# Performance work log

Hardware: AMD Instinct MI355X
Metric: run time of the kernel (lower is better)

## Reference

```python
import jax, jax.numpy as jnp
import numpy as np


def setup_inputs() -> dict:
    key = jax.random.key(0)
    ks = jax.random.split(key, 7)
    B, T, D, H, C = 256, 512, 128, 512, 10
    s_ih = 1.0 / np.sqrt(H)
    return {
        "X": jax.random.normal(ks[0], (B, T, D), dtype=jnp.float32),
        "W_ih": jax.random.normal(ks[1], (4 * H, D), dtype=jnp.float32) * s_ih,
        "W_hh": jax.random.normal(ks[2], (4 * H, H), dtype=jnp.float32) * s_ih,
        "b_ih": jax.random.normal(ks[3], (4 * H,), dtype=jnp.float32) * s_ih,
        "b_hh": jax.random.normal(ks[4], (4 * H,), dtype=jnp.float32) * s_ih,
        "W_lin": jax.random.normal(ks[5], (C, H), dtype=jnp.float32) * s_ih,
        "b_lin": jax.random.normal(ks[6], (C,), dtype=jnp.float32) * s_ih,
    }


def _lstm_mean_h(X, W_ih, W_hh, b_ih, b_hh):
    B, T, D = X.shape
    H = W_hh.shape[1]
    # Input projections for all timesteps at once: [T, B, 4H]
    x_proj = jnp.einsum("btd,kd->tbk", X, W_ih) + b_ih + b_hh

    def step(carry, xp):
        h, c = carry
        gates = xp + h @ W_hh.T  # [B, 4H]
        i, f, g, o = jnp.split(gates, 4, axis=-1)  # PyTorch i,f,g,o order
        i = jax.nn.sigmoid(i)
        f = jax.nn.sigmoid(f)
        g = jnp.tanh(g)
        o = jax.nn.sigmoid(o)
        c = f * c + i * g
        h = o * jnp.tanh(c)
        return (h, c), h

    h0 = jnp.zeros((B, H), dtype=X.dtype)
    (_, _), hs = jax.lax.scan(step, (h0, h0), x_proj)  # hs: [T, B, H]
    return jnp.mean(hs, axis=0)  # == sum(h_t)/T


def reference(X, W_ih, W_hh, b_ih, b_hh, W_lin, b_lin):
    states = _lstm_mean_h(X, W_ih, W_hh, b_ih, b_hh)  # [B, H]
    logits = states @ W_lin.T + b_lin  # [B, num_classes]
    return logits
```

## Files before the change

kernel.cpp:

```cpp
#include <hip/hip_runtime.h>
#include <stdint.h>


#define T_STEPS 512
#define BATCH   256
#define DIM     128
#define HID     512
#define NGRP    16
#define BT      16

typedef _Float16 half8 __attribute__((ext_vector_type(8)));
typedef _Float16 half4 __attribute__((ext_vector_type(4)));
typedef float    f32x4 __attribute__((ext_vector_type(4)));

#define HBUF_HALFS (2 * BATCH * HID)
#define FLG_OFF    (HBUF_HALFS * 2)
#define WS_NEEDED  (FLG_OFF + NGRP * 128)

__device__ __forceinline__ half8 cvt8(f32x4 a, f32x4 b) {
  half8 r;
  r[0]=(_Float16)a[0]; r[1]=(_Float16)a[1]; r[2]=(_Float16)a[2]; r[3]=(_Float16)a[3];
  r[4]=(_Float16)b[0]; r[5]=(_Float16)b[1]; r[6]=(_Float16)b[2]; r[7]=(_Float16)b[3];
  return r;
}
__device__ __forceinline__ half8 load8_cvt(const float* p) {
  const f32x4* q = (const f32x4*)p;
  return cvt8(q[0], q[1]);
}
__device__ __forceinline__ float fsig(float x) {
  return __builtin_amdgcn_rcpf(1.f + __expf(-x));
}
__device__ __forceinline__ float ftanh(float x) {
  return 1.f - 2.f * __builtin_amdgcn_rcpf(1.f + __expf(2.f * x));
}

union h4u { unsigned long long u; half4 h; };
union h8u { unsigned long long u2[2]; half8 h; };

__global__ __launch_bounds__(256, 1) void lstm_persistent(
    const float* __restrict__ X,   const float* __restrict__ Wih,
    const float* __restrict__ Whh, const float* __restrict__ bih,
    const float* __restrict__ bhh, const float* __restrict__ Wlin,
    float* __restrict__ out, _Float16* __restrict__ hbuf,
    unsigned* __restrict__ flg)
{
  const int tid  = threadIdx.x;
  const int w    = tid >> 6;
  const int lane = tid & 63;
  const int col  = lane & 15;
  const int q    = lane >> 4;
  const int bid  = blockIdx.x;
  const int g    = bid & 15;
  const int blk  = bid >> 4;
  const int J    = blk * 64 + w * 16;
  const int wid  = blk * 4 + w;
  const int b_my = g * BT + col;

  half8 whh[16][4];
  half8 wih[4][4];
  #pragma unroll
  for (int kc = 0; kc < 16; ++kc)
    #pragma unroll
    for (int mt = 0; mt < 4; ++mt) {
      const int row = mt * HID + J + col;
      whh[kc][mt] = load8_cvt(Whh + (size_t)row * HID + kc * 32 + q * 8);
    }
  #pragma unroll
  for (int xc = 0; xc < 4; ++xc)
    #pragma unroll
    for (int mt = 0; mt < 4; ++mt) {
      const int row = mt * HID + J + col;
      wih[xc][mt] = load8_cvt(Wih + (size_t)row * DIM + xc * 32 + q * 8);
    }

  float bias[4][4], c_st[4], hsum[4];
  #pragma unroll
  for (int mt = 0; mt < 4; ++mt)
    #pragma unroll
    for (int r = 0; r < 4; ++r) {
      const int row = mt * HID + J + q * 4 + r;
      bias[mt][r] = bih[row] + bhh[row];
    }
  #pragma unroll
  for (int r = 0; r < 4; ++r) { c_st[r] = 0.f; hsum[r] = 0.f; }

  unsigned* myflg = flg + g * 32;
  const float* Xb = X + (size_t)b_my * T_STEPS * DIM;

  f32x4 xraw[8];
  #pragma unroll
  for (int xc = 0; xc < 4; ++xc) {
    const f32x4* p = (const f32x4*)(Xb + xc * 32 + q * 8);
    xraw[2 * xc] = p[0]; xraw[2 * xc + 1] = p[1];
  }
  f32x4 acc[4];
  #pragma unroll
  for (int mt = 0; mt < 4; ++mt) acc[mt] = (f32x4){0.f, 0.f, 0.f, 0.f};
  #pragma unroll
  for (int xc = 0; xc < 4; ++xc) {
    half8 xb = cvt8(xraw[2 * xc], xraw[2 * xc + 1]);
    #pragma unroll
    for (int mt = 0; mt < 4; ++mt)
      acc[mt] = __builtin_amdgcn_mfma_f32_16x16x32_f16(wih[xc][mt], xb, acc[mt], 0, 0, 0);
  }

  for (int t = 0; t < T_STEPS; ++t) {
    {
      const int tn = (t + 1 < T_STEPS) ? (t + 1) : (T_STEPS - 1);
      const float* xp = Xb + (size_t)tn * DIM + q * 8;
      #pragma unroll
      for (int xc = 0; xc < 4; ++xc) {
        const f32x4* src = (const f32x4*)(xp + xc * 32);
        xraw[2 * xc]     = src[0];
        xraw[2 * xc + 1] = src[1];
      }
    }

    if (t > 0) {
      const unsigned target = (unsigned)t;
      for (;;) {
        unsigned v = __hip_atomic_load(myflg + (lane & 31), __ATOMIC_RELAXED,
                                       __HIP_MEMORY_SCOPE_AGENT);
        if (__all((int)(v >= target))) break;
      }
      __builtin_amdgcn_sched_barrier(0);

      const unsigned long long* hp =
          (const unsigned long long*)(hbuf + (size_t)(t & 1) * (BATCH * HID)
                                      + (size_t)b_my * HID) + q * 2;
      unsigned long long lo[16], hi[16];
      #pragma unroll
      for (int kc = 0; kc < 16; ++kc) {
        lo[kc] = __hip_atomic_load(hp + kc * 8,     __ATOMIC_RELAXED, __HIP_MEMORY_SCOPE_AGENT);
        hi[kc] = __hip_atomic_load(hp + kc * 8 + 1, __ATOMIC_RELAXED, __HIP_MEMORY_SCOPE_AGENT);
      }
      #pragma unroll
      for (int kc = 0; kc < 16; ++kc) {
        h8u u; u.u2[0] = lo[kc]; u.u2[1] = hi[kc];
        #pragma unroll
        for (int mt = 0; mt < 4; ++mt)
          acc[mt] = __builtin_amdgcn_mfma_f32_16x16x32_f16(whh[kc][mt], u.h, acc[mt], 0, 0, 0);
      }
    }

    h4u hv;
    #pragma unroll
    for (int r = 0; r < 4; ++r) {
      const float ig = fsig(acc[0][r] + bias[0][r]);
      const float fg = fsig(acc[1][r] + bias[1][r]);
      const float gg = ftanh(acc[2][r] + bias[2][r]);
      const float og = fsig(acc[3][r] + bias[3][r]);
      const float cc = fg * c_st[r] + ig * gg;
      c_st[r] = cc;
      const float h = og * ftanh(cc);
      hsum[r] += h;
      hv.h[r] = (_Float16)h;
    }
    unsigned long long* hw =
        (unsigned long long*)(hbuf + (size_t)((t + 1) & 1) * (BATCH * HID)
                              + (size_t)b_my * HID + J + q * 4);
    __hip_atomic_store(hw, hv.u, __ATOMIC_RELAXED, __HIP_MEMORY_SCOPE_AGENT);

    if (t + 1 < T_STEPS) {
      asm volatile("s_waitcnt vmcnt(0)" ::: "memory");
      if (lane == 0)
        __hip_atomic_store(myflg + wid, (unsigned)(t + 1), __ATOMIC_RELAXED,
                           __HIP_MEMORY_SCOPE_AGENT);

      #pragma unroll
      for (int mt = 0; mt < 4; ++mt) acc[mt] = (f32x4){0.f, 0.f, 0.f, 0.f};
      #pragma unroll
      for (int xc = 0; xc < 4; ++xc) {
        half8 xb = cvt8(xraw[2 * xc], xraw[2 * xc + 1]);
        #pragma unroll
        for (int mt = 0; mt < 4; ++mt)
          acc[mt] = __builtin_amdgcn_mfma_f32_16x16x32_f16(wih[xc][mt], xb, acc[mt], 0, 0, 0);
      }
    }
  }

  const float inv = 1.0f / (float)T_STEPS;
  float m[4];
  #pragma unroll
  for (int r = 0; r < 4; ++r) m[r] = hsum[r] * inv;
  #pragma unroll
  for (int cls = 0; cls < 10; ++cls) {
    f32x4 wl = *(const f32x4*)(Wlin + (size_t)cls * HID + J + q * 4);
    float p = m[0] * wl[0] + m[1] * wl[1] + m[2] * wl[2] + m[3] * wl[3];
    p += __shfl_xor(p, 16, 64);
    p += __shfl_xor(p, 32, 64);
    if (q == 0) atomicAdd(out + b_my * 10 + cls, p);
  }
}

__global__ void init_out(const float* __restrict__ blin, float* __restrict__ out) {
  const int i = blockIdx.x * blockDim.x + threadIdx.x;
  if (i < BATCH * 10) out[i] = blin[i % 10];
}

extern "C" void kernel_launch(void* const* d_in, const int* in_sizes, int n_in,
                              void* d_out, int out_size, void* d_ws, size_t ws_size,
                              hipStream_t stream) {
  const float* X    = (const float*)d_in[0];
  const float* Wih  = (const float*)d_in[1];
  const float* Whh  = (const float*)d_in[2];
  const float* bih  = (const float*)d_in[3];
  const float* bhh  = (const float*)d_in[4];
  const float* Wlin = (const float*)d_in[5];
  const float* blin = (const float*)d_in[6];
  float* out = (float*)d_out;

  if (ws_size < (size_t)WS_NEEDED) return;

  _Float16* hbuf = (_Float16*)d_ws;
  unsigned* flg  = (unsigned*)((char*)d_ws + FLG_OFF);

  hipMemsetAsync(d_ws, 0, WS_NEEDED, stream);
  init_out<<<10, 256, 0, stream>>>(blin, out);
  lstm_persistent<<<128, 256, 0, stream>>>(X, Wih, Whh, bih, bhh, Wlin, out,
                                           hbuf, flg);
}
```

Baseline: 3.329 ms.

## Replace flag-based step sync with sentinel-tagged ring buffer of hidden states

```diff
diff --git a/kernel.cpp b/kernel.cpp
--- a/kernel.cpp
+++ b/kernel.cpp
@@ -8,14 +8,15 @@
 #define HID     512
 #define NGRP    16
 #define BT      16
+#define RBUF    8
 
 typedef _Float16 half8 __attribute__((ext_vector_type(8)));
 typedef _Float16 half4 __attribute__((ext_vector_type(4)));
 typedef float    f32x4 __attribute__((ext_vector_type(4)));
 
-#define HBUF_HALFS (2 * BATCH * HID)
-#define FLG_OFF    (HBUF_HALFS * 2)
-#define WS_NEEDED  (FLG_OFF + NGRP * 128)
+#define SLOT_HALFS (BATCH * HID)
+#define WS_NEEDED  (RBUF * SLOT_HALFS * 2)
+#define SENT       0x7F7F7F7F7F7F7F7FULL
 
 __device__ __forceinline__ half8 cvt8(f32x4 a, f32x4 b) {
   half8 r;
@@ -41,8 +42,7 @@
     const float* __restrict__ X,   const float* __restrict__ Wih,
     const float* __restrict__ Whh, const float* __restrict__ bih,
     const float* __restrict__ bhh, const float* __restrict__ Wlin,
-    float* __restrict__ out, _Float16* __restrict__ hbuf,
-    unsigned* __restrict__ flg)
+    float* __restrict__ out, _Float16* __restrict__ hbuf)
 {
   const int tid  = threadIdx.x;
   const int w    = tid >> 6;
@@ -53,7 +53,6 @@
   const int g    = bid & 15;
   const int blk  = bid >> 4;
   const int J    = blk * 64 + w * 16;
-  const int wid  = blk * 4 + w;
   const int b_my = g * BT + col;
 
   half8 whh[16][4];
@@ -84,8 +83,8 @@
   #pragma unroll
   for (int r = 0; r < 4; ++r) { c_st[r] = 0.f; hsum[r] = 0.f; }
 
-  unsigned* myflg = flg + g * 32;
   const float* Xb = X + (size_t)b_my * T_STEPS * DIM;
+  const size_t pub_off = (size_t)b_my * HID + J + q * 4;
 
   f32x4 xraw[8];
   #pragma unroll
@@ -116,24 +115,32 @@
       }
     }
 
+    {
+      unsigned long long* rp = (unsigned long long*)
+          (hbuf + (size_t)((t + 3) & (RBUF - 1)) * SLOT_HALFS + pub_off);
+      __hip_atomic_store(rp, (unsigned long long)SENT, __ATOMIC_RELAXED,
+                         __HIP_MEMORY_SCOPE_AGENT);
+    }
+
     if (t > 0) {
-      const unsigned target = (unsigned)t;
+      const unsigned long long* hp = (const unsigned long long*)
+          (hbuf + (size_t)(t & (RBUF - 1)) * SLOT_HALFS
+                 + (size_t)b_my * HID) + q * 2;
+      unsigned long long lo[16], hi[16];
       for (;;) {
-        unsigned v = __hip_atomic_load(myflg + (lane & 31), __ATOMIC_RELAXED,
-                                       __HIP_MEMORY_SCOPE_AGENT);
-        if (__all((int)(v >= target))) break;
+        #pragma unroll
+        for (int kc = 0; kc < 16; ++kc) {
+          lo[kc] = __hip_atomic_load(hp + kc * 8,     __ATOMIC_RELAXED, __HIP_MEMORY_SCOPE_AGENT);
+          hi[kc] = __hip_atomic_load(hp + kc * 8 + 1, __ATOMIC_RELAXED, __HIP_MEMORY_SCOPE_AGENT);
+        }
+        int ok = 1;
+        #pragma unroll
+        for (int kc = 0; kc < 16; ++kc)
+          ok &= (int)(lo[kc] != SENT) & (int)(hi[kc] != SENT);
+        if (__all(ok)) break;
       }
       __builtin_amdgcn_sched_barrier(0);
 
-      const unsigned long long* hp =
-          (const unsigned long long*)(hbuf + (size_t)(t & 1) * (BATCH * HID)
-                                      + (size_t)b_my * HID) + q * 2;
-      unsigned long long lo[16], hi[16];
-      #pragma unroll
-      for (int kc = 0; kc < 16; ++kc) {
-        lo[kc] = __hip_atomic_load(hp + kc * 8,     __ATOMIC_RELAXED, __HIP_MEMORY_SCOPE_AGENT);
-        hi[kc] = __hip_atomic_load(hp + kc * 8 + 1, __ATOMIC_RELAXED, __HIP_MEMORY_SCOPE_AGENT);
-      }
       #pragma unroll
       for (int kc = 0; kc < 16; ++kc) {
         h8u u; u.u2[0] = lo[kc]; u.u2[1] = hi[kc];
@@ -156,17 +163,15 @@
       hsum[r] += h;
       hv.h[r] = (_Float16)h;
     }
-    unsigned long long* hw =
-        (unsigned long long*)(hbuf + (size_t)((t + 1) & 1) * (BATCH * HID)
-                              + (size_t)b_my * HID + J + q * 4);
-    __hip_atomic_store(hw, hv.u, __ATOMIC_RELAXED, __HIP_MEMORY_SCOPE_AGENT);
+
+    asm volatile("s_waitcnt vmcnt(0)" ::: "memory");
+    {
+      unsigned long long* hw = (unsigned long long*)
+          (hbuf + (size_t)((t + 1) & (RBUF - 1)) * SLOT_HALFS + pub_off);
+      __hip_atomic_store(hw, hv.u, __ATOMIC_RELAXED, __HIP_MEMORY_SCOPE_AGENT);
+    }
 
     if (t + 1 < T_STEPS) {
-      asm volatile("s_waitcnt vmcnt(0)" ::: "memory");
-      if (lane == 0)
-        __hip_atomic_store(myflg + wid, (unsigned)(t + 1), __ATOMIC_RELAXED,
-                           __HIP_MEMORY_SCOPE_AGENT);
-
       #pragma unroll
       for (int mt = 0; mt < 4; ++mt) acc[mt] = (f32x4){0.f, 0.f, 0.f, 0.f};
       #pragma unroll
@@ -213,10 +218,9 @@
   if (ws_size < (size_t)WS_NEEDED) return;
 
   _Float16* hbuf = (_Float16*)d_ws;
-  unsigned* flg  = (unsigned*)((char*)d_ws + FLG_OFF);
-
-  hipMemsetAsync(d_ws, 0, WS_NEEDED, stream);
+
+  hipMemsetAsync(d_ws, 0x7F, WS_NEEDED, stream);
   init_out<<<10, 256, 0, stream>>>(blin, out);
   lstm_persistent<<<128, 256, 0, stream>>>(X, Wih, Whh, bih, bhh, Wlin, out,
-                                           hbuf, flg);
-}
+                                           hbuf);
+}
```

Measured after the change: 4.233 ms. 27.2% more time.

## Interleave two batch sub-groups per block to hide recurrent sync latency

Applied to the files above, without the earlier changes.

```diff
diff --git a/kernel.cpp b/kernel.cpp
--- a/kernel.cpp
+++ b/kernel.cpp
@@ -6,16 +6,15 @@
 #define BATCH   256
 #define DIM     128
 #define HID     512
-#define NGRP    16
-#define BT      16
+#define NGRP    8
 
 typedef _Float16 half8 __attribute__((ext_vector_type(8)));
-typedef _Float16 half4 __attribute__((ext_vector_type(4)));
 typedef float    f32x4 __attribute__((ext_vector_type(4)));
-
-#define HBUF_HALFS (2 * BATCH * HID)
-#define FLG_OFF    (HBUF_HALFS * 2)
-#define WS_NEEDED  (FLG_OFF + NGRP * 128)
+typedef float    f32x2 __attribute__((ext_vector_type(2)));
+
+#define SLOT_HALFS (BATCH * HID)
+#define FLG_OFF    (2 * SLOT_HALFS * 2)
+#define WS_NEEDED  (FLG_OFF + NGRP * 2 * 64 * 4)
 
 __device__ __forceinline__ half8 cvt8(f32x4 a, f32x4 b) {
   half8 r;
@@ -34,8 +33,113 @@
   return 1.f - 2.f * __builtin_amdgcn_rcpf(1.f + __expf(2.f * x));
 }
 
-union h4u { unsigned long long u; half4 h; };
+union h2u { unsigned u; _Float16 h[2]; };
 union h8u { unsigned long long u2[2]; half8 h; };
+
+template<int S>
+__device__ __forceinline__ void phase(
+    const int t, const int lane, const int q, const int J, const int wid,
+    const int bMy, const int bOth,
+    const half8 (&whh)[16][2], const half8 (&wih)[4][2],
+    const float (&bias)[2][4],
+    f32x4 (&acc)[2], float (&c_st)[2], float (&hsum)[2],
+    f32x4 (&xraw)[8], const float* __restrict__ Xb,
+    _Float16* __restrict__ hbuf,
+    unsigned* __restrict__ flgMine, unsigned* __restrict__ flgOth,
+    unsigned long long (&lo)[16], unsigned long long (&hi)[16])
+{
+  const int  tgt     = (S == 0) ? t : (t + 1);
+  const bool doPoll  = (S == 0) ? (t >= 1) : (t + 1 < T_STEPS);
+  const bool notLast = (t + 1 < T_STEPS);
+
+  unsigned ev = 0xFFFFFFFFu;
+  if (doPoll)
+    ev = __hip_atomic_load(flgOth + lane, __ATOMIC_RELAXED,
+                           __HIP_MEMORY_SCOPE_AGENT);
+
+  if (t > 0) {
+    #pragma unroll
+    for (int kc = 0; kc < 16; ++kc) {
+      h8u u; u.u2[0] = lo[kc]; u.u2[1] = hi[kc];
+      acc[0] = __builtin_amdgcn_mfma_f32_16x16x32_f16(whh[kc][0], u.h, acc[0], 0, 0, 0);
+      acc[1] = __builtin_amdgcn_mfma_f32_16x16x32_f16(whh[kc][1], u.h, acc[1], 0, 0, 0);
+    }
+  }
+
+  h2u hv;
+  {
+    const float i0 = fsig (acc[0][0] + bias[0][0]);
+    const float f0 = fsig (acc[0][1] + bias[0][1]);
+    const float g0 = ftanh(acc[1][0] + bias[1][0]);
+    const float o0 = fsig (acc[1][1] + bias[1][1]);
+    const float c0 = f0 * c_st[0] + i0 * g0;
+    c_st[0] = c0;
+    const float h0 = o0 * ftanh(c0);
+    hsum[0] += h0;
+    const float i1 = fsig (acc[0][2] + bias[0][2]);
+    const float f1 = fsig (acc[0][3] + bias[0][3]);
+    const float g1 = ftanh(acc[1][2] + bias[1][2]);
+    const float o1 = fsig (acc[1][3] + bias[1][3]);
+    const float c1 = f1 * c_st[1] + i1 * g1;
+    c_st[1] = c1;
+    const float h1 = o1 * ftanh(c1);
+    hsum[1] += h1;
+    hv.h[0] = (_Float16)h0; hv.h[1] = (_Float16)h1;
+  }
+
+  if (notLast) {
+    unsigned* hw = (unsigned*)(hbuf + (size_t)((t + 1) & 1) * SLOT_HALFS
+                               + (size_t)bMy * HID + J + 2 * q);
+    __hip_atomic_store(hw, hv.u, __ATOMIC_RELAXED, __HIP_MEMORY_SCOPE_AGENT);
+  }
+
+  if (doPoll) {
+    if (!__all((int)(ev >= (unsigned)tgt))) {
+      for (;;) {
+        unsigned v = __hip_atomic_load(flgOth + lane, __ATOMIC_RELAXED,
+                                       __HIP_MEMORY_SCOPE_AGENT);
+        if (__all((int)(v >= (unsigned)tgt))) break;
+      }
+    }
+    __builtin_amdgcn_sched_barrier(0);
+  }
+
+  if (notLast) {
+    asm volatile("s_waitcnt vmcnt(0)" ::: "memory");
+    if (lane == 0)
+      __hip_atomic_store(flgMine + wid, (unsigned)(t + 1), __ATOMIC_RELAXED,
+                         __HIP_MEMORY_SCOPE_AGENT);
+  }
+
+  if (doPoll) {
+    const unsigned long long* hp = (const unsigned long long*)
+        (hbuf + (size_t)(tgt & 1) * SLOT_HALFS + (size_t)bOth * HID) + q * 2;
+    #pragma unroll
+    for (int kc = 0; kc < 16; ++kc) {
+      lo[kc] = __hip_atomic_load(hp + kc * 8,     __ATOMIC_RELAXED, __HIP_MEMORY_SCOPE_AGENT);
+      hi[kc] = __hip_atomic_load(hp + kc * 8 + 1, __ATOMIC_RELAXED, __HIP_MEMORY_SCOPE_AGENT);
+    }
+  }
+
+  if (notLast) {
+    #pragma unroll
+    for (int mt = 0; mt < 2; ++mt) acc[mt] = (f32x4){0.f, 0.f, 0.f, 0.f};
+    #pragma unroll
+    for (int xc = 0; xc < 4; ++xc) {
+      half8 xb = cvt8(xraw[2 * xc], xraw[2 * xc + 1]);
+      acc[0] = __builtin_amdgcn_mfma_f32_16x16x32_f16(wih[xc][0], xb, acc[0], 0, 0, 0);
+      acc[1] = __builtin_amdgcn_mfma_f32_16x16x32_f16(wih[xc][1], xb, acc[1], 0, 0, 0);
+    }
+    const int tn = (t + 2 < T_STEPS) ? (t + 2) : (T_STEPS - 1);
+    const float* xp = Xb + (size_t)tn * DIM + q * 8;
+    #pragma unroll
+    for (int xc = 0; xc < 4; ++xc) {
+      const f32x4* src = (const f32x4*)(xp + xc * 32);
+      xraw[2 * xc]     = src[0];
+      xraw[2 * xc + 1] = src[1];
+    }
+  }
+}
 
 __global__ __launch_bounds__(256, 1) void lstm_persistent(
     const float* __restrict__ X,   const float* __restrict__ Wih,
@@ -50,146 +154,102 @@
   const int col  = lane & 15;
   const int q    = lane >> 4;
   const int bid  = blockIdx.x;
-  const int g    = bid & 15;
-  const int blk  = bid >> 4;
-  const int J    = blk * 64 + w * 16;
+  const int g    = bid & 7;
+  const int blk  = bid >> 3;
+  const int J    = blk * 32 + w * 8;
   const int wid  = blk * 4 + w;
-  const int b_my = g * BT + col;
-
-  half8 whh[16][4];
-  half8 wih[4][4];
+  const int bA   = g * 32 + col;
+  const int bB   = g * 32 + 16 + col;
+
+  half8 whh[16][2];
+  half8 wih[4][2];
+  const int gpair = col & 1, uoff = col >> 1;
   #pragma unroll
   for (int kc = 0; kc < 16; ++kc)
     #pragma unroll
-    for (int mt = 0; mt < 4; ++mt) {
-      const int row = mt * HID + J + col;
+    for (int mt = 0; mt < 2; ++mt) {
+      const int row = (2 * mt + gpair) * HID + J + uoff;
       whh[kc][mt] = load8_cvt(Whh + (size_t)row * HID + kc * 32 + q * 8);
     }
   #pragma unroll
   for (int xc = 0; xc < 4; ++xc)
     #pragma unroll
-    for (int mt = 0; mt < 4; ++mt) {
-      const int row = mt * HID + J + col;
+    for (int mt = 0; mt < 2; ++mt) {
+      const int row = (2 * mt + gpair) * HID + J + uoff;
       wih[xc][mt] = load8_cvt(Wih + (size_t)row * DIM + xc * 32 + q * 8);
     }
 
-  float bias[4][4], c_st[4], hsum[4];
-  #pragma unroll
-  for (int mt = 0; mt < 4; ++mt)
+  float bias[2][4];
+  #pragma unroll
+  for (int mt = 0; mt < 2; ++mt)
     #pragma unroll
     for (int r = 0; r < 4; ++r) {
-      const int row = mt * HID + J + q * 4 + r;
+      const int row = (2 * mt + (r & 1)) * HID + J + 2 * q + (r >> 1);
       bias[mt][r] = bih[row] + bhh[row];
     }
-  #pragma unroll
-  for (int r = 0; r < 4; ++r) { c_st[r] = 0.f; hsum[r] = 0.f; }
-
-  unsigned* myflg = flg + g * 32;
-  const float* Xb = X + (size_t)b_my * T_STEPS * DIM;
-
-  f32x4 xraw[8];
+
+  float cA[2] = {0.f, 0.f}, cB[2] = {0.f, 0.f};
+  float hsA[2] = {0.f, 0.f}, hsB[2] = {0.f, 0.f};
+  const float* XbA = X + (size_t)bA * T_STEPS * DIM;
+  const float* XbB = X + (size_t)bB * T_STEPS * DIM;
+  unsigned* flgA = flg + (g * 2 + 0) * 64;
+  unsigned* flgB = flg + (g * 2 + 1) * 64;
+
+  f32x4 xrA[8], xrB[8];
   #pragma unroll
   for (int xc = 0; xc < 4; ++xc) {
-    const f32x4* p = (const f32x4*)(Xb + xc * 32 + q * 8);
-    xraw[2 * xc] = p[0]; xraw[2 * xc + 1] = p[1];
-  }
-  f32x4 acc[4];
-  #pragma unroll
-  for (int mt = 0; mt < 4; ++mt) acc[mt] = (f32x4){0.f, 0.f, 0.f, 0.f};
+    const f32x4* pa = (const f32x4*)(XbA + xc * 32 + q * 8);
+    const f32x4* pb = (const f32x4*)(XbB + xc * 32 + q * 8);
+    xrA[2 * xc] = pa[0]; xrA[2 * xc + 1] = pa[1];
+    xrB[2 * xc] = pb[0]; xrB[2 * xc + 1] = pb[1];
+  }
+  f32x4 accA[2], accB[2];
+  #pragma unroll
+  for (int mt = 0; mt < 2; ++mt) {
+    accA[mt] = (f32x4){0.f, 0.f, 0.f, 0.f};
+    accB[mt] = (f32x4){0.f, 0.f, 0.f, 0.f};
+  }
   #pragma unroll
   for (int xc = 0; xc < 4; ++xc) {
-    half8 xb = cvt8(xraw[2 * xc], xraw[2 * xc + 1]);
-    #pragma unroll
-    for (int mt = 0; mt < 4; ++mt)
-      acc[mt] = __builtin_amdgcn_mfma_f32_16x16x32_f16(wih[xc][mt], xb, acc[mt], 0, 0, 0);
-  }
+    half8 xa = cvt8(xrA[2 * xc], xrA[2 * xc + 1]);
+    half8 xb = cvt8(xrB[2 * xc], xrB[2 * xc + 1]);
+    #pragma unroll
+    for (int mt = 0; mt < 2; ++mt) {
+      accA[mt] = __builtin_amdgcn_mfma_f32_16x16x32_f16(wih[xc][mt], xa, accA[mt], 0, 0, 0);
+      accB[mt] = __builtin_amdgcn_mfma_f32_16x16x32_f16(wih[xc][mt], xb, accB[mt], 0, 0, 0);
+    }
+  }
+  #pragma unroll
+  for (int xc = 0; xc < 4; ++xc) {
+    const f32x4* pa = (const f32x4*)(XbA + (size_t)DIM + xc * 32 + q * 8);
+    const f32x4* pb = (const f32x4*)(XbB + (size_t)DIM + xc * 32 + q * 8);
+    xrA[2 * xc] = pa[0]; xrA[2 * xc + 1] = pa[1];
+    xrB[2 * xc] = pb[0]; xrB[2 * xc + 1] = pb[1];
+  }
+
+  unsigned long long lo[16], hi[16];
 
   for (int t = 0; t < T_STEPS; ++t) {
-    {
-      const int tn = (t + 1 < T_STEPS) ? (t + 1) : (T_STEPS - 1);
-      const float* xp = Xb + (size_t)tn * DIM + q * 8;
-      #pragma unroll
-      for (int xc = 0; xc < 4; ++xc) {
-        const f32x4* src = (const f32x4*)(xp + xc * 32);
-        xraw[2 * xc]     = src[0];
-        xraw[2 * xc + 1] = src[1];
-      }
-    }
-
-    if (t > 0) {
-      const unsigned target = (unsigned)t;
-      for (;;) {
-        unsigned v = __hip_atomic_load(myflg + (lane & 31), __ATOMIC_RELAXED,
-                                       __HIP_MEMORY_SCOPE_AGENT);
-        if (__all((int)(v >= target))) break;
-      }
-      __builtin_amdgcn_sched_barrier(0);
-
-      const unsigned long long* hp =
-          (const unsigned long long*)(hbuf + (size_t)(t & 1) * (BATCH * HID)
-                                      + (size_t)b_my * HID) + q * 2;
-      unsigned long long lo[16], hi[16];
-      #pragma unroll
-      for (int kc = 0; kc < 16; ++kc) {
-        lo[kc] = __hip_atomic_load(hp + kc * 8,     __ATOMIC_RELAXED, __HIP_MEMORY_SCOPE_AGENT);
-        hi[kc] = __hip_atomic_load(hp + kc * 8 + 1, __ATOMIC_RELAXED, __HIP_MEMORY_SCOPE_AGENT);
-      }
-      #pragma unroll
-      for (int kc = 0; kc < 16; ++kc) {
-        h8u u; u.u2[0] = lo[kc]; u.u2[1] = hi[kc];
-        #pragma unroll
-        for (int mt = 0; mt < 4; ++mt)
-          acc[mt] = __builtin_amdgcn_mfma_f32_16x16x32_f16(whh[kc][mt], u.h, acc[mt], 0, 0, 0);
-      }
-    }
-
-    h4u hv;
-    #pragma unroll
-    for (int r = 0; r < 4; ++r) {
-      const float ig = fsig(acc[0][r] + bias[0][r]);
-      const float fg = fsig(acc[1][r] + bias[1][r]);
-      const float gg = ftanh(acc[2][r] + bias[2][r]);
-      const float og = fsig(acc[3][r] + bias[3][r]);
-      const float cc = fg * c_st[r] + ig * gg;
-      c_st[r] = cc;
-      const float h = og * ftanh(cc);
-      hsum[r] += h;
-      hv.h[r] = (_Float16)h;
-    }
-    unsigned long long* hw =
-        (unsigned long long*)(hbuf + (size_t)((t + 1) & 1) * (BATCH * HID)
-                              + (size_t)b_my * HID + J + q * 4);
-    __hip_atomic_store(hw, hv.u, __ATOMIC_RELAXED, __HIP_MEMORY_SCOPE_AGENT);
-
-    if (t + 1 < T_STEPS) {
-      asm volatile("s_waitcnt vmcnt(0)" ::: "memory");
-      if (lane == 0)
-        __hip_atomic_store(myflg + wid, (unsigned)(t + 1), __ATOMIC_RELAXED,
-                           __HIP_MEMORY_SCOPE_AGENT);
-
-      #pragma unroll
-      for (int mt = 0; mt < 4; ++mt) acc[mt] = (f32x4){0.f, 0.f, 0.f, 0.f};
-      #pragma unroll
-      for (int xc = 0; xc < 4; ++xc) {
-        half8 xb = cvt8(xraw[2 * xc], xraw[2 * xc + 1]);
-        #pragma unroll
-        for (int mt = 0; mt < 4; ++mt)
-          acc[mt] = __builtin_amdgcn_mfma_f32_16x16x32_f16(wih[xc][mt], xb, acc[mt], 0, 0, 0);
-      }
-    }
+    phase<0>(t, lane, q, J, wid, bA, bB, whh, wih, bias,
+             accA, cA, hsA, xrA, XbA, hbuf, flgA, flgB, lo, hi);
+    phase<1>(t, lane, q, J, wid, bB, bA, whh, wih, bias,
+             accB, cB, hsB, xrB, XbB, hbuf, flgB, flgA, lo, hi);
   }
 
   const float inv = 1.0f / (float)T_STEPS;
-  float m[4];
-  #pragma unroll
-  for (int r = 0; r < 4; ++r) m[r] = hsum[r] * inv;
   #pragma unroll
   for (int cls = 0; cls < 10; ++cls) {
-    f32x4 wl = *(const f32x4*)(Wlin + (size_t)cls * HID + J + q * 4);
-    float p = m[0] * wl[0] + m[1] * wl[1] + m[2] * wl[2] + m[3] * wl[3];
-    p += __shfl_xor(p, 16, 64);
-    p += __shfl_xor(p, 32, 64);
-    if (q == 0) atomicAdd(out + b_my * 10 + cls, p);
+    const f32x2 wl = *(const f32x2*)(Wlin + (size_t)cls * HID + J + 2 * q);
+    float pA = (hsA[0] * wl[0] + hsA[1] * wl[1]) * inv;
+    float pB = (hsB[0] * wl[0] + hsB[1] * wl[1]) * inv;
+    pA += __shfl_xor(pA, 16, 64);
+    pA += __shfl_xor(pA, 32, 64);
+    pB += __shfl_xor(pB, 16, 64);
+    pB += __shfl_xor(pB, 32, 64);
+    if (q == 0) {
+      atomicAdd(out + bA * 10 + cls, pA);
+      atomicAdd(out + bB * 10 + cls, pB);
+    }
   }
 }
 
@@ -215,7 +275,7 @@
   _Float16* hbuf = (_Float16*)d_ws;
   unsigned* flg  = (unsigned*)((char*)d_ws + FLG_OFF);
 
-  hipMemsetAsync(d_ws, 0, WS_NEEDED, stream);
+  hipMemsetAsync((char*)d_ws + FLG_OFF, 0, NGRP * 2 * 64 * 4, stream);
   init_out<<<10, 256, 0, stream>>>(blin, out);
   lstm_persistent<<<128, 256, 0, stream>>>(X, Wih, Whh, bih, bhh, Wlin, out,
                                            hbuf, flg);
```

Result: slower. 5.895 ms (+77.1%).

## Use per-block flags and share h-state loads across waves via LDS

Applied to the files above, without the earlier changes.

```diff
diff --git a/kernel.cpp b/kernel.cpp
--- a/kernel.cpp
+++ b/kernel.cpp
@@ -12,10 +12,11 @@
 typedef _Float16 half8 __attribute__((ext_vector_type(8)));
 typedef _Float16 half4 __attribute__((ext_vector_type(4)));
 typedef float    f32x4 __attribute__((ext_vector_type(4)));
-
-#define HBUF_HALFS (2 * BATCH * HID)
-#define FLG_OFF    (HBUF_HALFS * 2)
-#define WS_NEEDED  (FLG_OFF + NGRP * 128)
+typedef unsigned u32x4 __attribute__((ext_vector_type(4)));
+
+#define SLOT_HALFS (BATCH * HID)
+#define FLG_OFF    (2 * SLOT_HALFS * 2)
+#define WS_NEEDED  (FLG_OFF + NGRP * 8 * 128)
 
 __device__ __forceinline__ half8 cvt8(f32x4 a, f32x4 b) {
   half8 r;
@@ -35,7 +36,7 @@
 }
 
 union h4u { unsigned long long u; half4 h; };
-union h8u { unsigned long long u2[2]; half8 h; };
+union c16 { unsigned long long u2[2]; u32x4 v; };
 
 __global__ __launch_bounds__(256, 1) void lstm_persistent(
     const float* __restrict__ X,   const float* __restrict__ Wih,
@@ -44,6 +45,8 @@
     float* __restrict__ out, _Float16* __restrict__ hbuf,
     unsigned* __restrict__ flg)
 {
+  __shared__ unsigned hsh[4096];
+
   const int tid  = threadIdx.x;
   const int w    = tid >> 6;
   const int lane = tid & 63;
@@ -53,7 +56,6 @@
   const int g    = bid & 15;
   const int blk  = bid >> 4;
   const int J    = blk * 64 + w * 16;
-  const int wid  = blk * 4 + w;
   const int b_my = g * BT + col;
 
   half8 whh[16][4];
@@ -84,62 +86,83 @@
   #pragma unroll
   for (int r = 0; r < 4; ++r) { c_st[r] = 0.f; hsum[r] = 0.f; }
 
-  unsigned* myflg = flg + g * 32;
+  unsigned* gflg = flg + g * 8 * 32;
   const float* Xb = X + (size_t)b_my * T_STEPS * DIM;
 
-  f32x4 xraw[8];
+  f32x4 xr0[8], xr1[8];
   #pragma unroll
   for (int xc = 0; xc < 4; ++xc) {
     const f32x4* p = (const f32x4*)(Xb + xc * 32 + q * 8);
-    xraw[2 * xc] = p[0]; xraw[2 * xc + 1] = p[1];
+    xr0[2 * xc] = p[0]; xr0[2 * xc + 1] = p[1];
   }
   f32x4 acc[4];
   #pragma unroll
   for (int mt = 0; mt < 4; ++mt) acc[mt] = (f32x4){0.f, 0.f, 0.f, 0.f};
   #pragma unroll
   for (int xc = 0; xc < 4; ++xc) {
-    half8 xb = cvt8(xraw[2 * xc], xraw[2 * xc + 1]);
+    half8 xb = cvt8(xr0[2 * xc], xr0[2 * xc + 1]);
     #pragma unroll
     for (int mt = 0; mt < 4; ++mt)
       acc[mt] = __builtin_amdgcn_mfma_f32_16x16x32_f16(wih[xc][mt], xb, acc[mt], 0, 0, 0);
   }
+  #pragma unroll
+  for (int xc = 0; xc < 4; ++xc) {
+    const f32x4* p1 = (const f32x4*)(Xb + (size_t)1 * DIM + xc * 32 + q * 8);
+    const f32x4* p2 = (const f32x4*)(Xb + (size_t)2 * DIM + xc * 32 + q * 8);
+    xr1[2 * xc] = p1[0]; xr1[2 * xc + 1] = p1[1];
+    xr0[2 * xc] = p2[0]; xr0[2 * xc + 1] = p2[1];
+  }
 
   for (int t = 0; t < T_STEPS; ++t) {
-    {
-      const int tn = (t + 1 < T_STEPS) ? (t + 1) : (T_STEPS - 1);
-      const float* xp = Xb + (size_t)tn * DIM + q * 8;
-      #pragma unroll
-      for (int xc = 0; xc < 4; ++xc) {
-        const f32x4* src = (const f32x4*)(xp + xc * 32);
-        xraw[2 * xc]     = src[0];
-        xraw[2 * xc + 1] = src[1];
-      }
-    }
-
     if (t > 0) {
-      const unsigned target = (unsigned)t;
-      for (;;) {
-        unsigned v = __hip_atomic_load(myflg + (lane & 31), __ATOMIC_RELAXED,
-                                       __HIP_MEMORY_SCOPE_AGENT);
-        if (__all((int)(v >= target))) break;
+      {
+        const int fl = lane & 7;
+        for (;;) {
+          unsigned v = __hip_atomic_load(gflg + fl * 32, __ATOMIC_RELAXED,
+                                         __HIP_MEMORY_SCOPE_AGENT);
+          if (fl == blk) v = 0xFFFFFFFFu;
+          if (__all((int)(v >= (unsigned)t))) break;
+        }
       }
       __builtin_amdgcn_sched_barrier(0);
 
-      const unsigned long long* hp =
-          (const unsigned long long*)(hbuf + (size_t)(t & 1) * (BATCH * HID)
-                                      + (size_t)b_my * HID) + q * 2;
-      unsigned long long lo[16], hi[16];
+      unsigned long long lo[4], hi[4];
+      {
+        const unsigned long long* base = (const unsigned long long*)
+            (hbuf + (size_t)(t & 1) * SLOT_HALFS + (size_t)b_my * HID);
+        #pragma unroll
+        for (int i = 0; i < 4; ++i) {
+          const int kc = w * 4 + i;
+          lo[i] = __hip_atomic_load(base + kc * 8 + q * 2,     __ATOMIC_RELAXED, __HIP_MEMORY_SCOPE_AGENT);
+          hi[i] = __hip_atomic_load(base + kc * 8 + q * 2 + 1, __ATOMIC_RELAXED, __HIP_MEMORY_SCOPE_AGENT);
+        }
+      }
+      #pragma unroll
+      for (int i = 0; i < 4; ++i) {
+        const int kc = w * 4 + i;
+        c16 u; u.u2[0] = lo[i]; u.u2[1] = hi[i];
+        *(u32x4*)(hsh + kc * 256 + col * 16 + q * 4) = u.v;
+      }
+      __syncthreads();
+
+      {
+        const int tn = (t + 2 < T_STEPS) ? (t + 2) : (T_STEPS - 1);
+        const float* xp = Xb + (size_t)tn * DIM + q * 8;
+        f32x4* dst = (t & 1) ? xr1 : xr0;
+        #pragma unroll
+        for (int xc = 0; xc < 4; ++xc) {
+          const f32x4* src = (const f32x4*)(xp + xc * 32);
+          dst[2 * xc]     = src[0];
+          dst[2 * xc + 1] = src[1];
+        }
+      }
+
       #pragma unroll
       for (int kc = 0; kc < 16; ++kc) {
-        lo[kc] = __hip_atomic_load(hp + kc * 8,     __ATOMIC_RELAXED, __HIP_MEMORY_SCOPE_AGENT);
-        hi[kc] = __hip_atomic_load(hp + kc * 8 + 1, __ATOMIC_RELAXED, __HIP_MEMORY_SCOPE_AGENT);
-      }
-      #pragma unroll
-      for (int kc = 0; kc < 16; ++kc) {
-        h8u u; u.u2[0] = lo[kc]; u.u2[1] = hi[kc];
+        const half8 hb = *(const half8*)(hsh + kc * 256 + col * 16 + q * 4);
         #pragma unroll
         for (int mt = 0; mt < 4; ++mt)
-          acc[mt] = __builtin_amdgcn_mfma_f32_16x16x32_f16(whh[kc][mt], u.h, acc[mt], 0, 0, 0);
+          acc[mt] = __builtin_amdgcn_mfma_f32_16x16x32_f16(whh[kc][mt], hb, acc[mt], 0, 0, 0);
       }
     }
 
@@ -156,22 +179,24 @@
       hsum[r] += h;
       hv.h[r] = (_Float16)h;
     }
-    unsigned long long* hw =
-        (unsigned long long*)(hbuf + (size_t)((t + 1) & 1) * (BATCH * HID)
-                              + (size_t)b_my * HID + J + q * 4);
-    __hip_atomic_store(hw, hv.u, __ATOMIC_RELAXED, __HIP_MEMORY_SCOPE_AGENT);
 
     if (t + 1 < T_STEPS) {
-      asm volatile("s_waitcnt vmcnt(0)" ::: "memory");
-      if (lane == 0)
-        __hip_atomic_store(myflg + wid, (unsigned)(t + 1), __ATOMIC_RELAXED,
-                           __HIP_MEMORY_SCOPE_AGENT);
+      unsigned long long* hw =
+          (unsigned long long*)(hbuf + (size_t)((t + 1) & 1) * SLOT_HALFS
+                                + (size_t)b_my * HID + J + q * 4);
+      __hip_atomic_store(hw, hv.u, __ATOMIC_RELAXED, __HIP_MEMORY_SCOPE_AGENT);
+
+      __syncthreads();
+      if (tid == 0)
+        __hip_atomic_store(gflg + blk * 32, (unsigned)(t + 1),
+                           __ATOMIC_RELAXED, __HIP_MEMORY_SCOPE_AGENT);
 
       #pragma unroll
       for (int mt = 0; mt < 4; ++mt) acc[mt] = (f32x4){0.f, 0.f, 0.f, 0.f};
+      const f32x4* xbuf = ((t + 1) & 1) ? xr1 : xr0;
       #pragma unroll
       for (int xc = 0; xc < 4; ++xc) {
-        half8 xb = cvt8(xraw[2 * xc], xraw[2 * xc + 1]);
+        half8 xb = cvt8(xbuf[2 * xc], xbuf[2 * xc + 1]);
         #pragma unroll
         for (int mt = 0; mt < 4; ++mt)
           acc[mt] = __builtin_amdgcn_mfma_f32_16x16x32_f16(wih[xc][mt], xb, acc[mt], 0, 0, 0);
@@ -215,7 +240,7 @@
   _Float16* hbuf = (_Float16*)d_ws;
   unsigned* flg  = (unsigned*)((char*)d_ws + FLG_OFF);
 
-  hipMemsetAsync(d_ws, 0, WS_NEEDED, stream);
+  hipMemsetAsync((char*)d_ws + FLG_OFF, 0, NGRP * 8 * 128, stream);
   init_out<<<10, 256, 0, stream>>>(blin, out);
   lstm_persistent<<<128, 256, 0, stream>>>(X, Wih, Whh, bih, bhh, Wlin, out,
                                            hbuf, flg);
```

Result: faster. 2.832 ms (-14.9%).
